# Optimization experiments

Measured on AMD Instinct MI355X. Metric: run time of the kernel, lower is better.

Reference implementation:

```python
import jax, jax.numpy as jnp
import numpy as np

ADJ = np.array([[0,1,0,0,0,0],[1,0,1,0,1,0],[0,1,0,1,0,0],[0,0,1,0,0,0],[0,1,0,0,0,1],[0,0,0,0,1,0]])
EDGES = np.stack(np.nonzero(ADJ), axis=1)  # [10,2] row-major, same order as torch.nonzero
UPPER = (1, 2, 3, 4)
N_PART = 6
B, H, W = 1, 96, 96


def conv1x1(x, w):
    return jnp.einsum('bchw,oc->bohw', x, w)


def affine(x, s, b):  # InPlaceABNSync(activation='none'), eval mode with stats folded into scale/bias
    return x * s[None, :, None, None] + b[None, :, None, None]


def bilinear(x, py, px):  # x [B,C,H,W]; py,px [B,H,W]; zero padding outside
    Hh, Ww = x.shape[2], x.shape[3]
    def samp(img, py, px):
        y0 = jnp.floor(py); x0 = jnp.floor(px)
        wy = py - y0; wx = px - x0
        def get(yi, xi):
            valid = ((yi >= 0) & (yi < Hh) & (xi >= 0) & (xi < Ww)).astype(img.dtype)
            yc = jnp.clip(yi, 0, Hh - 1).astype(jnp.int32)
            xc = jnp.clip(xi, 0, Ww - 1).astype(jnp.int32)
            return img[:, yc, xc] * valid
        return (get(y0, x0) * (1 - wy) * (1 - wx) + get(y0, x0 + 1) * (1 - wy) * wx
                + get(y0 + 1, x0) * wy * (1 - wx) + get(y0 + 1, x0 + 1) * wy * wx)
    return jax.vmap(samp)(x, py, px)


def dfconv(x, ow, ob, w):
    # modulated deformable conv v2 (DCNv2), 3x3, stride 1, pad 1, 1 deformable group
    o = jax.lax.conv_general_dilated(x, ow, (1, 1), 'SAME',
            dimension_numbers=('NCHW', 'OIHW', 'NCHW')) + ob[None, :, None, None]
    off, mask = o[:, :18], jax.nn.sigmoid(o[:, 18:27])
    Hh, Ww = x.shape[2], x.shape[3]
    yy, xx = jnp.meshgrid(jnp.arange(Hh, dtype=x.dtype), jnp.arange(Ww, dtype=x.dtype), indexing='ij')
    out = jnp.zeros((x.shape[0], w.shape[0], Hh, Ww), x.dtype)
    for k in range(9):  # fixed 3x3 taps
        py = yy[None] + (k // 3 - 1) + off[:, 2 * k]
        px = xx[None] + (k % 3 - 1) + off[:, 2 * k + 1]
        s = bilinear(x, py, px) * mask[:, k:k + 1]
        out = out + jnp.einsum('bchw,oc->bohw', s, w[:, :, k // 3, k % 3])
    return out


def gru_cell(x, h, wih, bih, whh, bhh):  # Conv2dGRU cell, 1x1 kernel, single step
    gi = conv1x1(x, wih) + bih[None, :, None, None]
    gh = conv1x1(h, whh) + bhh[None, :, None, None]
    i_r, i_z, i_n = jnp.split(gi, 3, axis=1)
    h_r, h_z, h_n = jnp.split(gh, 3, axis=1)
    r = jax.nn.sigmoid(i_r + h_r)
    z = jax.nn.sigmoid(i_z + h_z)
    n = jnp.tanh(i_n + r * h_n)
    return (1 - z) * n + z * h


def _forward(p_fea, xp, xh, dp_ow1, dp_ob1, dp_w1, dp_s1, dp_b1, dp_ow2, dp_ob2, dp_w2, dp_s2, dp_b2,
             dp_aw, dp_ab, dp_bw, dp_bb, dc_w1, dc_s1, dc_b1, dc_w2, dc_b2, dc_wfh, dc_sfh, dc_bfh,
             gru_wih1, gru_bih1, gru_whh1, gru_bhh1, gru_wih2, gru_bih2, gru_whh2, gru_bhh2):
    # Part_Dependency per directed edge (A -> B)
    per_node = [[] for _ in range(N_PART)]
    for e in range(EDGES.shape[0]):
        a, b = int(EDGES[e, 0]), int(EDGES[e, 1])
        pA, pB = xp[a], xp[b]
        h = jax.nn.relu(affine(dfconv(jnp.concatenate([p_fea, pA], 1), dp_ow1[e], dp_ob1[e], dp_w1[e]), dp_s1[e], dp_b1[e]))
        h = jax.nn.relu(affine(dfconv(h, dp_ow2[e], dp_ob2[e], dp_w2[e]), dp_s2[e], dp_b2[e]))
        A_att = jax.nn.sigmoid(conv1x1(pA, dp_aw[e]) + dp_ab[e][None, :, None, None])
        B_att = jax.nn.sigmoid(conv1x1(pB, dp_bw[e]) + dp_bb[e][None, :, None, None])
        per_node[b].append((1 - A_att) * h * B_att)
    # max-aggregation of incoming messages per part node
    xpp = [m[0] if len(m) == 1 else jnp.max(jnp.stack(m, -1), -1) for m in per_node]
    # decomp: half-node -> part-node messages, then sum
    msgs = []
    for j in range(N_PART):
        hf = xh[0] if (j + 1) in UPPER else xh[1]
        cat = jnp.concatenate([hf, xp[j]], 1)
        a_ = jax.nn.relu(affine(conv1x1(cat, dc_w1[j]), dc_s1[j], dc_b1[j]))
        att = jax.nn.sigmoid(conv1x1(a_, dc_w2[j]) + dc_b2[j][None, :, None, None])
        xhp = jax.nn.relu(affine(conv1x1(att * p_fea, dc_wfh[j]), dc_sfh[j], dc_bfh[j]))
        msgs.append(xpp[j] + xhp)
    # per-node 2-layer Conv2dGRU update (seq len 1, h0 = 0); take layer-2 hidden
    xp_out = []
    h0 = jnp.zeros_like(xp[0])
    for j in range(N_PART):
        xin = jnp.concatenate([xp[j], msgs[j]], 1)
        h1 = gru_cell(xin, h0, gru_wih1[j], gru_bih1[j], gru_whh1[j], gru_bhh1[j])
        h2 = gru_cell(h1, h0, gru_wih2[j], gru_bih2[j], gru_whh2[j], gru_bhh2[j])
        xp_out.append(h2)
    return jnp.stack(xp_out, 0), jnp.stack(msgs, 0)


def setup_inputs():
    ks = iter(jax.random.split(jax.random.key(0), 64))
    nrm = lambda shape, s: jax.random.normal(next(ks), shape, jnp.float32) * s
    HD, IN, E = 10, 256, EDGES.shape[0]
    N = N_PART
    return {
        'p_fea': nrm((B, IN, H, W), 1.0),
        'xp': nrm((N, B, HD, H, W), 1.0),
        'xh': nrm((2, B, HD, H, W), 1.0),
        'dp_ow1': nrm((E, 27, IN + HD, 3, 3), 0.005), 'dp_ob1': nrm((E, 27), 0.01),
        'dp_w1': nrm((E, 2 * HD, IN + HD, 3, 3), 0.02),
        'dp_s1': jnp.ones((E, 2 * HD), jnp.float32), 'dp_b1': jnp.zeros((E, 2 * HD), jnp.float32),
        'dp_ow2': nrm((E, 27, 2 * HD, 3, 3), 0.02), 'dp_ob2': nrm((E, 27), 0.01),
        'dp_w2': nrm((E, HD, 2 * HD, 3, 3), 0.07),
        'dp_s2': jnp.ones((E, HD), jnp.float32), 'dp_b2': jnp.zeros((E, HD), jnp.float32),
        'dp_aw': nrm((E, 1, HD), 0.3), 'dp_ab': jnp.zeros((E, 1), jnp.float32),
        'dp_bw': nrm((E, 1, HD), 0.3), 'dp_bb': jnp.zeros((E, 1), jnp.float32),
        'dc_w1': nrm((N, 2 * HD, 2 * HD), 0.2),
        'dc_s1': jnp.ones((N, 2 * HD), jnp.float32), 'dc_b1': jnp.zeros((N, 2 * HD), jnp.float32),
        'dc_w2': nrm((N, 1, 2 * HD), 0.2), 'dc_b2': jnp.zeros((N, 1), jnp.float32),
        'dc_wfh': nrm((N, HD, IN), 0.06),
        'dc_sfh': jnp.ones((N, HD), jnp.float32), 'dc_bfh': jnp.zeros((N, HD), jnp.float32),
        'gru_wih1': nrm((N, 3 * HD, 2 * HD), 0.2), 'gru_bih1': jnp.zeros((N, 3 * HD), jnp.float32),
        'gru_whh1': nrm((N, 3 * HD, HD), 0.3), 'gru_bhh1': jnp.zeros((N, 3 * HD), jnp.float32),
        'gru_wih2': nrm((N, 3 * HD, HD), 0.3), 'gru_bih2': jnp.zeros((N, 3 * HD), jnp.float32),
        'gru_whh2': nrm((N, 3 * HD, HD), 0.3), 'gru_bhh2': jnp.zeros((N, 3 * HD), jnp.float32),
    }


def reference(p_fea, xp, xh, dp_ow1, dp_ob1, dp_w1, dp_s1, dp_b1, dp_ow2, dp_ob2, dp_w2, dp_s2, dp_b2,
              dp_aw, dp_ab, dp_bw, dp_bb, dc_w1, dc_s1, dc_b1, dc_w2, dc_b2, dc_wfh, dc_sfh, dc_bfh,
              gru_wih1, gru_bih1, gru_whh1, gru_bhh1, gru_wih2, gru_bih2, gru_whh2, gru_bhh2):
    return _forward(p_fea, xp, xh, dp_ow1, dp_ob1, dp_w1, dp_s1, dp_b1, dp_ow2, dp_ob2, dp_w2, dp_s2, dp_b2,
                    dp_aw, dp_ab, dp_bw, dp_bb, dc_w1, dc_s1, dc_b1, dc_w2, dc_b2, dc_wfh, dc_sfh, dc_bfh,
                    gru_wih1, gru_bih1, gru_whh1, gru_bhh1, gru_wih2, gru_bih2, gru_whh2, gru_bhh2)
```

## Files before the change

### kernel.cpp

```cpp
#include <hip/hip_runtime.h>
#include <hip/hip_bf16.h>

#define DEV static __device__ __forceinline__

DEV float sigm(float x) { return 1.f / (1.f + __expf(-x)); }

typedef __attribute__((ext_vector_type(8))) short s8;
typedef __attribute__((ext_vector_type(4))) float f4;
typedef _Float16 h4 __attribute__((ext_vector_type(4)));

DEV unsigned short f2bf(float f) {
  unsigned u = __float_as_uint(f);
  return (unsigned short)((u + 0x7FFFu + ((u >> 16) & 1u)) >> 16);
}
DEV float bf2f(unsigned short h) { return __uint_as_float(((unsigned)h) << 16); }

__constant__ int d_esrc[10] = {0,1,1,1,2,2,3,4,4,5};
__constant__ int d_inc[6][3] = {{1,-1,-1},{0,4,7},{2,6,-1},{5,-1,-1},{3,9,-1},{8,-1,-1}};
__constant__ int d_ne[6] = {1,3,2,1,2,1};

#define TW 32
#define TH 8
#define SW 41
#define SDC 40
#define SH 16
#define SN 656

DEV void prep_w_body(const float* src, float* dst, int OC, int C,
                     int tap_major, int total, int i) {
  if (i >= total) return;
  int t = i % 9; int n = i / 9;
  int c = n % C; n /= C;
  int oc = n % OC; int e = n / OC;
  float v = src[i];
  int inner = tap_major ? (t * C + c) : (c * 9 + t);
  dst[(e * C * 9 + inner) * OC + oc] = v;
}

__global__ void prep_all_k(const float* __restrict__ dp_ow2, float* __restrict__ wf2,
                           const float* __restrict__ dp_w2, float* __restrict__ wm2,
                           const float* __restrict__ dp_ow1,
                           unsigned short* __restrict__ aw1,
                           const float* __restrict__ dp_w1,
                           unsigned short* __restrict__ awY,
                           unsigned short* __restrict__ awU, int use_u) {
  int b = blockIdx.x;
  if (b < 190) {
    prep_w_body(dp_ow2, wf2, 27, 20, 0, 48600, b * 256 + threadIdx.x);
  } else if (b < 261) {
    prep_w_body(dp_w2, wm2, 10, 20, 1, 18000, (b - 190) * 256 + threadIdx.x);
  } else if (b < 926) {
    if (use_u) return;
    int i = (b - 261) * 256 + threadIdx.x;
    if (i >= 170240) return;
    int lane = i & 63;
    int tile = (i >> 6) & 1;
    int cg = (i >> 7) % 133;
    int e = (i >> 7) / 133;
    int m = lane & 15, quad = lane >> 4;
    int oc = tile * 16 + m;
    unsigned short* out = aw1 + ((e * 133 + cg) * 2 + tile) * 1024 + lane * 16;
#pragma unroll
    for (int j = 0; j < 8; ++j) {
      int k = quad * 8 + j;
      int csel = k >> 4, t = k & 15;
      int c = 2 * cg + csel;
      float w = (oc < 27 && t < 9) ? dp_ow1[((e * 27 + oc) * 266 + c) * 9 + t] : 0.f;
      unsigned short h = f2bf(w);
      out[j] = h;
      out[8 + j] = f2bf(w - bf2f(h));
    }
  } else if (b < 1196) {
    if (use_u) return;
    int i = (b - 926) * 256 + threadIdx.x;
    int lane = i & 63;
    int grp = i >> 6;
    int mt = grp % 12;
    int ks = (grp / 12) % 9;
    int e = grp / 108;
    int m16 = lane & 15, quad = lane >> 4;
    int M = mt * 16 + m16;
    unsigned short* out = awY + ((e * 9 + ks) * 12 + mt) * 1024 + lane * 16;
#pragma unroll
    for (int j = 0; j < 8; ++j) {
      int c = ks * 32 + quad * 8 + j;
      float w = 0.f;
      if (M < 180 && c < 266) {
        int tap = M / 20, oc = M % 20;
        w = dp_w1[((e * 20 + oc) * 266 + c) * 9 + tap];
      }
      unsigned short h = f2bf(w);
      out[j] = h;
      out[8 + j] = f2bf(w - bf2f(h));
    }
  } else {
    if (!use_u) return;
    int i = (b - 1196) * 256 + threadIdx.x;
    int lane = i & 63;
    int grp = i >> 6;
    int mt = grp % 28;
    int ks = (grp / 28) % 9;
    int e = grp / 252;
    int m16 = lane & 15, quad = lane >> 4;
    int M = mt * 16 + m16;
    unsigned short* out = awU + ((e * 9 + ks) * 28 + mt) * 1024 + lane * 16;
#pragma unroll
    for (int j = 0; j < 8; ++j) {
      int c = ks * 32 + quad * 8 + j;
      float w = 0.f;
      if (c < 266) {
        if (M < 180) {
          int tap = M / 20, oc = M % 20;
          w = dp_w1[((e * 20 + oc) * 266 + c) * 9 + tap];
        } else if (M >= 192 && M < 435) {
          int u = M - 192, tap = u / 27, oc = u % 27;
          w = dp_ow1[((e * 27 + oc) * 266 + c) * 9 + tap];
        }
      }
      unsigned short h = f2bf(w);
      out[j] = h;
      out[8 + j] = f2bf(w - bf2f(h));
    }
  }
}

__global__ __launch_bounds__(256) void xt_k(
    const float* __restrict__ pfea, const float* __restrict__ xp,
    unsigned short* __restrict__ Xt_p, unsigned short* __restrict__ Xt_x) {
  __shared__ unsigned int lds[256][17];
  const int q0 = blockIdx.x * 256, yb = blockIdx.y;
  const int t = threadIdx.x;
  if (yb < 8) {
    const int c0 = yb * 32;
#pragma unroll
    for (int cc = 0; cc < 32; cc += 2) {
      float v0 = pfea[(c0 + cc) * 9216 + q0 + t];
      float v1 = pfea[(c0 + cc + 1) * 9216 + q0 + t];
      lds[t][cc >> 1] = (unsigned)f2bf(v0) | ((unsigned)f2bf(v1) << 16);
    }
    __syncthreads();
    unsigned int* dst = (unsigned int*)(Xt_p + (size_t)(q0 + t) * 256 + c0);
#pragma unroll
    for (int u = 0; u < 16; ++u) dst[u] = lds[t][u];
  } else {
    const int node = yb - 8;
#pragma unroll
    for (int cc = 0; cc < 32; cc += 2) {
      float v0 = (cc < 10) ? xp[(node * 10 + cc) * 9216 + q0 + t] : 0.f;
      float v1 = (cc + 1 < 10) ? xp[(node * 10 + cc + 1) * 9216 + q0 + t] : 0.f;
      lds[t][cc >> 1] = (unsigned)f2bf(v0) | ((unsigned)f2bf(v1) << 16);
    }
    __syncthreads();
    unsigned int* dst = (unsigned int*)(Xt_x + ((size_t)node * 9216 + q0 + t) * 32);
#pragma unroll
    for (int u = 0; u < 16; ++u) dst[u] = lds[t][u];
  }
}

__global__ void init2_k(const float* __restrict__ ob, float* __restrict__ o2,
                        float* __restrict__ h2) {
  int i = blockIdx.x * 256 + threadIdx.x;
  if (i < 2488320) o2[i] = ob[i / 9216];
  else h2[i - 2488320] = 0.f;
}

DEV int stage_goff(int i, int ty0, int tx0) {
  int r = i / SW, cl = i % SW;
  cl = min(cl, SDC - 1);
  int gy = min(max(ty0 - 4 + r, 0), 95);
  int gx = min(max(tx0 - 4 + cl, 0), 95);
  return gy * 96 + gx;
}

__global__ __launch_bounds__(256) void uni_gemm_k(
    const unsigned short* __restrict__ Xt_p,
    const unsigned short* __restrict__ Xt_x,
    const unsigned short* __restrict__ awU, unsigned short* __restrict__ Yg,
    unsigned short* __restrict__ Ug) {
  const int pxg = blockIdx.x, z = blockIdx.y, e = blockIdx.z;
  const int tid = threadIdx.x;
  const int lane = tid & 63, wv = tid >> 6;
  const int quad = lane >> 4, n16 = lane & 15;
  const unsigned short* xtx = Xt_x + (size_t)d_esrc[e] * 9216 * 32;
  const int qbase = pxg * 256 + wv * 64;
  int q[4];
#pragma unroll
  for (int nt = 0; nt < 4; ++nt) q[nt] = qbase + nt * 16 + n16;

  f4 acc[4][4] = {};

  for (int ks = 0; ks < 9; ++ks) {
    s8 Ah[4], Al[4];
#pragma unroll
    for (int mt = 0; mt < 4; ++mt) {
      const unsigned short* ap =
          awU + (((size_t)e * 9 + ks) * 28 + z * 4 + mt) * 1024 + lane * 16;
      Ah[mt] = *(const s8*)ap;
      Al[mt] = *(const s8*)(ap + 8);
    }
    s8 B[4];
    if (ks < 8) {
      const int co = ks * 32 + quad * 8;
#pragma unroll
      for (int nt = 0; nt < 4; ++nt)
        B[nt] = *(const s8*)(Xt_p + (size_t)q[nt] * 256 + co);
    } else {
      const int co = quad * 8;
#pragma unroll
      for (int nt = 0; nt < 4; ++nt)
        B[nt] = *(const s8*)(xtx + (size_t)q[nt] * 32 + co);
    }
#pragma unroll
    for (int nt = 0; nt < 4; ++nt)
#pragma unroll
      for (int mt = 0; mt < 4; ++mt) {
        acc[nt][mt] = __builtin_amdgcn_mfma_f32_16x16x32_bf16(Ah[mt], B[nt], acc[nt][mt], 0, 0, 0);
        acc[nt][mt] = __builtin_amdgcn_mfma_f32_16x16x32_bf16(Al[mt], B[nt], acc[nt][mt], 0, 0, 0);
      }
  }
  _Float16* Yh = (_Float16*)Yg;
  _Float16* Uh = (_Float16*)Ug;
#pragma unroll
  for (int nt = 0; nt < 4; ++nt) {
#pragma unroll
    for (int mt = 0; mt < 4; ++mt) {
      int m0 = (z * 4 + mt) * 16 + quad * 4;
      if (m0 < 180) {
        int tap = m0 / 20, oc0 = m0 - tap * 20;
        h4 v;
#pragma unroll
        for (int r = 0; r < 4; ++r) v[r] = (_Float16)acc[nt][mt][r];
        *(h4*)(Yh + (((size_t)(e * 9 + tap)) * 9216 + q[nt]) * 20 + oc0) = v;
      } else {
#pragma unroll
        for (int r = 0; r < 4; ++r) {
          int m = m0 + r;
          if (m >= 192 && m < 435)
            Uh[((size_t)e * 243 + (m - 192)) * 9216 + q[nt]] = (_Float16)acc[nt][mt][r];
        }
      }
    }
  }
}

__global__ __launch_bounds__(256) void shiftadd_k(
    const unsigned short* __restrict__ Ug, const float* __restrict__ ob,
    float* __restrict__ o1) {
  const int p = blockIdx.x * 256 + threadIdx.x;
  const int e = blockIdx.y;
  const int y = p / 96, x = p % 96;
  const _Float16* Uh = (const _Float16*)Ug;
  float acc[27];
#pragma unroll
  for (int oc = 0; oc < 27; ++oc) acc[oc] = ob[e * 27 + oc];
#pragma unroll
  for (int t = 0; t < 9; ++t) {
    int yy = y + t / 3 - 1, xx = x + t % 3 - 1;
    if (yy >= 0 && yy < 96 && xx >= 0 && xx < 96) {
      int q = yy * 96 + xx;
      const _Float16* up = Uh + ((size_t)e * 243 + t * 27) * 9216 + q;
#pragma unroll
      for (int oc = 0; oc < 27; ++oc)
        acc[oc] += (float)up[oc * 9216];
    }
  }
#pragma unroll
  for (int oc = 0; oc < 27; ++oc) o1[(e * 27 + oc) * 9216 + p] = acc[oc];
}

#define OSWB 35
#define OSEC 384
#define OBUF 896

__global__ __launch_bounds__(256) void offconv1_mfma_k(
    const float* __restrict__ pfea, const float* __restrict__ xp,
    const unsigned short* __restrict__ aw, const float* __restrict__ ob,
    float* __restrict__ o1) {
  __shared__ float sbuf[2][OBUF];
  const int e = blockIdx.x, m = blockIdx.y, z = blockIdx.z;
  const int tid = threadIdx.x;
  const int lane = tid & 63, wv = tid >> 6;
  const int quad = lane >> 4, n16 = lane & 15;
  const int tx0 = (m % 3) * 32, ty0 = (m / 3) * 8;
  const float* xpe = xp + d_esrc[e] * 10 * 9216;
  const int cg_lo = (z * 133) / 4, cg_hi = ((z + 1) * 133) / 4;

  int g[3]; bool oks[3];
#pragma unroll
  for (int i = 0; i < 3; ++i) {
    int s = tid + i * 256;
    int sec = s / OSEC, off = s - sec * OSEC;
    int r = off / OSWB, cl = off % OSWB;
    int gy = ty0 - 1 + r, gx = tx0 - 1 + cl;
    bool ok = (off < 350) && (cl < 34) && (gy >= 0) && (gy < 96) &&
              (gx >= 0) && (gx < 96);
    oks[i] = ok;
    g[i] = sec * 9216 + (ok ? (gy * 96 + gx) : 0);
  }
  if (tid < OBUF - 768) { sbuf[0][768 + tid] = 0.f; sbuf[1][768 + tid] = 0.f; }

  const int tbase = (quad & 1) * 8;
  const int csel = quad >> 1;
  int bdelta[8];
#pragma unroll
  for (int j = 0; j < 8; ++j) {
    int t = tbase + j;
    int dy = t / 3 - 1, dx = t % 3 - 1;
    bdelta[j] = csel * OSEC + dy * OSWB + dx;
  }
  int bidx[4];
#pragma unroll
  for (int nt = 0; nt < 4; ++nt) {
    int r = 2 * wv + (nt >> 1), h = nt & 1;
    bidx[nt] = (r + 1) * OSWB + (h * 16 + n16 + 1);
  }

  f4 acc[4][2] = {};

  int c0 = 2 * cg_lo;
  const float* base = (c0 < 256) ? (pfea + c0 * 9216) : (xpe + (c0 - 256) * 9216);
  float pv0 = oks[0] ? base[g[0]] : 0.f;
  float pv1 = oks[1] ? base[g[1]] : 0.f;
  float pv2 = oks[2] ? base[g[2]] : 0.f;

  int bsel = 0;
  for (int cg = cg_lo; cg < cg_hi; ++cg, bsel ^= 1) {
    float* buf = sbuf[bsel];
    buf[tid] = pv0; buf[tid + 256] = pv1; buf[tid + 512] = pv2;
    if (cg + 1 < cg_hi) {
      int c0n = 2 * (cg + 1);
      const float* nb = (c0n < 256) ? (pfea + c0n * 9216)
                                    : (xpe + (c0n - 256) * 9216);
      pv0 = oks[0] ? nb[g[0]] : 0.f;
      pv1 = oks[1] ? nb[g[1]] : 0.f;
      pv2 = oks[2] ? nb[g[2]] : 0.f;
    }
    const unsigned short* apc = aw + (e * 133 + cg) * 2048 + lane * 16;
    s8 Ah0 = *(const s8*)(apc);
    s8 Al0 = *(const s8*)(apc + 8);
    s8 Ah1 = *(const s8*)(apc + 1024);
    s8 Al1 = *(const s8*)(apc + 1024 + 8);
    __syncthreads();
#pragma unroll
    for (int nt = 0; nt < 4; ++nt) {
      union { s8 v; unsigned short u[8]; } Bh, Bl;
#pragma unroll
      for (int j = 0; j < 8; ++j) {
        float v = buf[bidx[nt] + bdelta[j]];
        unsigned short h = f2bf(v);
        Bh.u[j] = h;
        Bl.u[j] = f2bf(v - bf2f(h));
      }
      acc[nt][0] = __builtin_amdgcn_mfma_f32_16x16x32_bf16(Ah0, Bh.v, acc[nt][0], 0, 0, 0);
      acc[nt][0] = __builtin_amdgcn_mfma_f32_16x16x32_bf16(Ah0, Bl.v, acc[nt][0], 0, 0, 0);
      acc[nt][0] = __builtin_amdgcn_mfma_f32_16x16x32_bf16(Al0, Bh.v, acc[nt][0], 0, 0, 0);
      acc[nt][1] = __builtin_amdgcn_mfma_f32_16x16x32_bf16(Ah1, Bh.v, acc[nt][1], 0, 0, 0);
      acc[nt][1] = __builtin_amdgcn_mfma_f32_16x16x32_bf16(Ah1, Bl.v, acc[nt][1], 0, 0, 0);
      acc[nt][1] = __builtin_amdgcn_mfma_f32_16x16x32_bf16(Al1, Bh.v, acc[nt][1], 0, 0, 0);
    }
  }
#pragma unroll
  for (int nt = 0; nt < 4; ++nt) {
    int y = ty0 + 2 * wv + (nt >> 1);
    int xx = tx0 + (nt & 1) * 16 + n16;
    int p = y * 96 + xx;
#pragma unroll
    for (int t2 = 0; t2 < 2; ++t2)
#pragma unroll
      for (int r = 0; r < 4; ++r) {
        int oc = t2 * 16 + quad * 4 + r;
        if (oc < 27) {
          float v = acc[nt][t2][r];
          if (z == 0) v += ob[e * 27 + oc];
          atomicAdd(&o1[(e * 27 + oc) * 9216 + p], v);
        }
      }
  }
}

__global__ __launch_bounds__(256) void ygemm_k(
    const float* __restrict__ pfea, const float* __restrict__ xp,
    const unsigned short* __restrict__ awY, unsigned short* __restrict__ Yg) {
  const int pxg = blockIdx.x, z = blockIdx.y, e = blockIdx.z;
  const int tid = threadIdx.x;
  const int lane = tid & 63, wv = tid >> 6;
  const int quad = lane >> 4, n16 = lane & 15;
  const float* xpe = xp + d_esrc[e] * 10 * 9216;
  const int qbase = pxg * 256 + wv * 64;

  f4 acc[4][3] = {};

  for (int ks = 0; ks < 9; ++ks) {
    const int cq = ks * 32 + quad * 8;
    s8 Ah[3], Al[3];
#pragma unroll
    for (int mt = 0; mt < 3; ++mt) {
      const unsigned short* ap =
          awY + ((e * 9 + ks) * 12 + z * 3 + mt) * 1024 + lane * 16;
      Ah[mt] = *(const s8*)ap;
      Al[mt] = *(const s8*)(ap + 8);
    }
#pragma unroll
    for (int nt = 0; nt < 4; ++nt) {
      const int q = qbase + nt * 16 + n16;
      union { s8 v; unsigned short u[8]; } Bh, Bl;
#pragma unroll
      for (int j = 0; j < 8; ++j) {
        int c = cq + j;
        float v = 0.f;
        if (c < 256) v = pfea[c * 9216 + q];
        else if (c < 266) v = xpe[(c - 256) * 9216 + q];
        unsigned short h = f2bf(v);
        Bh.u[j] = h;
        Bl.u[j] = f2bf(v - bf2f(h));
      }
#pragma unroll
      for (int mt = 0; mt < 3; ++mt) {
        acc[nt][mt] = __builtin_amdgcn_mfma_f32_16x16x32_bf16(Ah[mt], Bh.v, acc[nt][mt], 0, 0, 0);
        acc[nt][mt] = __builtin_amdgcn_mfma_f32_16x16x32_bf16(Ah[mt], Bl.v, acc[nt][mt], 0, 0, 0);
        acc[nt][mt] = __builtin_amdgcn_mfma_f32_16x16x32_bf16(Al[mt], Bh.v, acc[nt][mt], 0, 0, 0);
      }
    }
  }
  _Float16* Yh = (_Float16*)Yg;
#pragma unroll
  for (int nt = 0; nt < 4; ++nt) {
    const int q = qbase + nt * 16 + n16;
#pragma unroll
    for (int mt = 0; mt < 3; ++mt)
#pragma unroll
      for (int r = 0; r < 4; ++r) {
        int m = z * 48 + mt * 16 + quad * 4 + r;
        if (m < 180) {
          int tap = m / 20, oc = m - tap * 20;
          Yh[((e * 9 + tap) * 9216 + q) * 20 + oc] = (_Float16)acc[nt][mt][r];
        }
      }
  }
}

__global__ __launch_bounds__(256) void dfgather_k(
    const float* __restrict__ o1, const unsigned short* __restrict__ Yg,
    float* __restrict__ h1a) {
  const int p = blockIdx.x * 256 + threadIdx.x;
  const int zt = blockIdx.y, e = blockIdx.z;
  const int y = p / 96, x = p % 96;
  float acc[20];
#pragma unroll
  for (int oc = 0; oc < 20; ++oc) acc[oc] = 0.f;

  const _Float16* Yh = (const _Float16*)Yg;
#pragma unroll
  for (int t = 0; t < 3; ++t) {
    const int k = zt * 3 + t;
    float offy = o1[(e * 27 + 2 * k) * 9216 + p];
    float offx = o1[(e * 27 + 2 * k + 1) * 9216 + p];
    float mk = sigm(o1[(e * 27 + 18 + k) * 9216 + p]);
    float py = (float)(y + k / 3 - 1) + offy;
    float px = (float)(x + k % 3 - 1) + offx;
    float fy = floorf(py), fx = floorf(px);
    float wy = py - fy, wx = px - fx;
    int iy = (int)fy, ix = (int)fx;
    const _Float16* yk = Yh + (size_t)(e * 9 + k) * 9216 * 20;
#pragma unroll
    for (int dy = 0; dy < 2; ++dy)
#pragma unroll
      for (int dx = 0; dx < 2; ++dx) {
        bool ok = (iy + dy >= 0) && (iy + dy < 96) && (ix + dx >= 0) && (ix + dx < 96);
        float cwc = (ok ? mk : 0.f) * (dy ? wy : (1.f - wy)) * (dx ? wx : (1.f - wx));
        int yc = min(max(iy + dy, 0), 95), xc = min(max(ix + dx, 0), 95);
        const h4* yp = (const h4*)(yk + (yc * 96 + xc) * 20);
#pragma unroll
        for (int g = 0; g < 5; ++g) {
          h4 v = yp[g];
#pragma unroll
          for (int u = 0; u < 4; ++u)
            acc[g * 4 + u] = fmaf(cwc, (float)v[u], acc[g * 4 + u]);
        }
      }
  }
#pragma unroll
  for (int oc = 0; oc < 20; ++oc)
    atomicAdd(&h1a[(e * 20 + oc) * 9216 + p], acc[oc]);
}

__global__ __launch_bounds__(256) void offconv2_k(
    const float* __restrict__ h1a, const float* __restrict__ wf,
    const float* __restrict__ s1, const float* __restrict__ b1,
    float* __restrict__ o2) {
  __shared__ float sbuf[2][2 * SN];
  const int e = blockIdx.x, m = blockIdx.y;
  const int c_lo = blockIdx.z * 10;
  const int tid = threadIdx.x;
  const int tx = tid % TW, ty = tid / TW;
  const int tx0 = (m % 3) * TW, ty0 = (m / 3) * TH;
  const int y = ty0 + ty, x = tx0 + tx;
  const int p = y * 96 + x;
  const float* base = h1a + e * 20 * 9216;

  const int g0 = stage_goff(tid, ty0, tx0);
  const int g1 = stage_goff(tid + 256, ty0, tx0);
  const int g2 = (tid < SN - 512) ? stage_goff(tid + 512, ty0, tx0) : 0;

  float vmask[9];
#pragma unroll
  for (int t = 0; t < 9; ++t) {
    int yy = y + t / 3 - 1, xx = x + t % 3 - 1;
    vmask[t] = ((yy >= 0) && (yy < 96) && (xx >= 0) && (xx < 96)) ? 1.f : 0.f;
  }
  const int vbase = (ty + 3) * SW + (tx + 3);

  float acc[27];
#pragma unroll
  for (int oc = 0; oc < 27; ++oc) acc[oc] = 0.f;

  const float* ia = base + c_lo * 9216;
  const float* ib = ia + 9216;
  float pa0 = ia[g0], pa1 = ia[g1], pa2 = (tid < SN - 512) ? ia[g2] : 0.f;
  float pb0 = ib[g0], pb1 = ib[g1], pb2 = (tid < SN - 512) ? ib[g2] : 0.f;

  int bsel = 0;
  for (int c = c_lo; c < c_lo + 10; c += 2, bsel ^= 1) {
    float sa = s1[e * 20 + c], ba = b1[e * 20 + c];
    float sb = s1[e * 20 + c + 1], bb2 = b1[e * 20 + c + 1];
    float* buf = sbuf[bsel];
    buf[tid] = fmaxf(fmaf(sa, pa0, ba), 0.f);
    buf[tid + 256] = fmaxf(fmaf(sa, pa1, ba), 0.f);
    if (tid < SN - 512) buf[tid + 512] = fmaxf(fmaf(sa, pa2, ba), 0.f);
    buf[SN + tid] = fmaxf(fmaf(sb, pb0, bb2), 0.f);
    buf[SN + tid + 256] = fmaxf(fmaf(sb, pb1, bb2), 0.f);
    if (tid < SN - 512) buf[SN + tid + 512] = fmaxf(fmaf(sb, pb2, bb2), 0.f);
    if (c + 2 < c_lo + 10) {
      const float* na = base + (c + 2) * 9216;
      const float* nb = base + (c + 3) * 9216;
      pa0 = na[g0]; pa1 = na[g1]; if (tid < SN - 512) pa2 = na[g2];
      pb0 = nb[g0]; pb1 = nb[g1]; if (tid < SN - 512) pb2 = nb[g2];
    }
    __syncthreads();
#pragma unroll
    for (int cc = 0; cc < 2; ++cc) {
      const float* wc = wf + (e * 20 + c + cc) * 243;
      const float* bp = buf + cc * SN;
#pragma unroll
      for (int t = 0; t < 9; ++t) {
        float v = vmask[t] * bp[vbase + (t / 3) * SW + (t % 3)];
#pragma unroll
        for (int oc = 0; oc < 27; ++oc)
          acc[oc] = fmaf(v, wc[t * 27 + oc], acc[oc]);
      }
    }
  }
#pragma unroll
  for (int oc = 0; oc < 27; ++oc)
    atomicAdd(&o2[(e * 27 + oc) * 9216 + p], acc[oc]);
}

__global__ __launch_bounds__(256) void dfmain2_k(
    const float* __restrict__ h1a, const float* __restrict__ o2,
    const float* __restrict__ wm, const float* __restrict__ s1,
    const float* __restrict__ b1, float* __restrict__ hout) {
  __shared__ float sbuf[2][2 * SN];
  const int e = blockIdx.x, m = blockIdx.y;
  const int c_lo = blockIdx.z * 10;
  const int tid = threadIdx.x;
  const int tx = tid % TW, ty = tid / TW;
  const int tx0 = (m % 3) * TW, ty0 = (m / 3) * TH;
  const int y = ty0 + ty, x = tx0 + tx;
  const int p = y * 96 + x;
  const float* base = h1a + e * 20 * 9216;

  const int g0 = stage_goff(tid, ty0, tx0);
  const int g1 = stage_goff(tid + 256, ty0, tx0);
  const int g2 = (tid < SN - 512) ? stage_goff(tid + 512, ty0, tx0) : 0;

  int iob[9]; float cw[9][4];
  bool oob = false;
#pragma unroll
  for (int k = 0; k < 9; ++k) {
    float offy = o2[(e * 27 + 2 * k) * 9216 + p];
    float offx = o2[(e * 27 + 2 * k + 1) * 9216 + p];
    float mk = sigm(o2[(e * 27 + 18 + k) * 9216 + p]);
    float py = (float)(y + k / 3 - 1) + offy;
    float px = (float)(x + k % 3 - 1) + offx;
    float fy = floorf(py), fx = floorf(px);
    float wy = py - fy, wx = px - fx;
    int iy = (int)fy, ix = (int)fx;
#pragma unroll
    for (int dy = 0; dy < 2; ++dy)
#pragma unroll
      for (int dx = 0; dx < 2; ++dx) {
        bool ok = (iy + dy >= 0) && (iy + dy < 96) && (ix + dx >= 0) && (ix + dx < 96);
        cw[k][dy * 2 + dx] =
            (ok ? mk : 0.f) * (dy ? wy : (1.f - wy)) * (dx ? wx : (1.f - wx));
      }
    int ir = iy - (ty0 - 4), ic = ix - (tx0 - 4);
    oob |= ((unsigned)ir > (unsigned)(SH - 2)) | ((unsigned)ic > (unsigned)(SDC - 2));
    iob[k] = min(max(ir, 0), SH - 2) * SW + min(max(ic, 0), SDC - 2);
  }

  float acc[10];
#pragma unroll
  for (int oc = 0; oc < 10; ++oc) acc[oc] = 0.f;

  const float* ia = base + c_lo * 9216;
  const float* ib = ia + 9216;
  float pa0 = ia[g0], pa1 = ia[g1], pa2 = (tid < SN - 512) ? ia[g2] : 0.f;
  float pb0 = ib[g0], pb1 = ib[g1], pb2 = (tid < SN - 512) ? ib[g2] : 0.f;

  int bsel = 0;
  for (int c = c_lo; c < c_lo + 10; c += 2, bsel ^= 1) {
    float sa = s1[e * 20 + c], ba = b1[e * 20 + c];
    float sb = s1[e * 20 + c + 1], bb2 = b1[e * 20 + c + 1];
    float* buf = sbuf[bsel];
    buf[tid] = fmaxf(fmaf(sa, pa0, ba), 0.f);
    buf[tid + 256] = fmaxf(fmaf(sa, pa1, ba), 0.f);
    if (tid < SN - 512) buf[tid + 512] = fmaxf(fmaf(sa, pa2, ba), 0.f);
    buf[SN + tid] = fmaxf(fmaf(sb, pb0, bb2), 0.f);
    buf[SN + tid + 256] = fmaxf(fmaf(sb, pb1, bb2), 0.f);
    if (tid < SN - 512) buf[SN + tid + 512] = fmaxf(fmaf(sb, pb2, bb2), 0.f);
    if (c + 2 < c_lo + 10) {
      const float* na = base + (c + 2) * 9216;
      const float* nb = base + (c + 3) * 9216;
      pa0 = na[g0]; pa1 = na[g1]; if (tid < SN - 512) pa2 = na[g2];
      pb0 = nb[g0]; pb1 = nb[g1]; if (tid < SN - 512) pb2 = nb[g2];
    }
    __syncthreads();
#pragma unroll
    for (int cc = 0; cc < 2; ++cc) {
      const float* bp = buf + cc * SN;
#pragma unroll
      for (int k = 0; k < 9; ++k) {
        const float* bk = bp + iob[k];
        float sv = cw[k][0] * bk[0] + cw[k][1] * bk[1] +
                   cw[k][2] * bk[SW] + cw[k][3] * bk[SW + 1];
        const float* wc = wm + ((e * 9 + k) * 20 + c + cc) * 10;
#pragma unroll
        for (int oc = 0; oc < 10; ++oc) acc[oc] = fmaf(sv, wc[oc], acc[oc]);
      }
    }
  }

  if (oob) {
#pragma unroll
    for (int oc = 0; oc < 10; ++oc) acc[oc] = 0.f;
    for (int k = 0; k < 9; ++k) {
      float offy = o2[(e * 27 + 2 * k) * 9216 + p];
      float offx = o2[(e * 27 + 2 * k + 1) * 9216 + p];
      float mk = sigm(o2[(e * 27 + 18 + k) * 9216 + p]);
      float py = (float)(y + k / 3 - 1) + offy;
      float px = (float)(x + k % 3 - 1) + offx;
      float fy = floorf(py), fx = floorf(px);
      float wy = py - fy, wx = px - fx;
      int iy = (int)fy, ix = (int)fx;
      int go[4]; float gw[4];
#pragma unroll
      for (int dy = 0; dy < 2; ++dy)
#pragma unroll
        for (int dx = 0; dx < 2; ++dx) {
          bool ok = (iy + dy >= 0) && (iy + dy < 96) && (ix + dx >= 0) && (ix + dx < 96);
          int yc = min(max(iy + dy, 0), 95), xc = min(max(ix + dx, 0), 95);
          go[dy * 2 + dx] = yc * 96 + xc;
          gw[dy * 2 + dx] =
              (ok ? mk : 0.f) * (dy ? wy : (1.f - wy)) * (dx ? wx : (1.f - wx));
        }
      for (int c = c_lo; c < c_lo + 10; ++c) {
        float sc = s1[e * 20 + c], bc = b1[e * 20 + c];
        const float* ptr = base + c * 9216;
        float v0 = fmaxf(fmaf(sc, ptr[go[0]], bc), 0.f);
        float v1 = fmaxf(fmaf(sc, ptr[go[1]], bc), 0.f);
        float v2 = fmaxf(fmaf(sc, ptr[go[2]], bc), 0.f);
        float v3 = fmaxf(fmaf(sc, ptr[go[3]], bc), 0.f);
        float sv = gw[0] * v0 + gw[1] * v1 + gw[2] * v2 + gw[3] * v3;
        const float* wc = wm + ((e * 9 + k) * 20 + c) * 10;
#pragma unroll
        for (int oc = 0; oc < 10; ++oc) acc[oc] = fmaf(sv, wc[oc], acc[oc]);
      }
    }
  }
#pragma unroll
  for (int oc = 0; oc < 10; ++oc)
    atomicAdd(&hout[(e * 10 + oc) * 9216 + p], acc[oc]);
}

__global__ __launch_bounds__(256) void conv_fh_k(
    const float* __restrict__ pfea, const float* __restrict__ wfh,
    float* __restrict__ accfh) {
  const int j = blockIdx.y;
  const int z = blockIdx.z;
  const int p = blockIdx.x * 256 + threadIdx.x;
  const int c_lo = z * 64;
  float acc[10];
#pragma unroll
  for (int c = 0; c < 10; ++c) acc[c] = 0.f;
  for (int ci = c_lo; ci < c_lo + 64; ci += 4) {
    float pv0 = pfea[ci * 9216 + p];
    float pv1 = pfea[(ci + 1) * 9216 + p];
    float pv2 = pfea[(ci + 2) * 9216 + p];
    float pv3 = pfea[(ci + 3) * 9216 + p];
#pragma unroll
    for (int c = 0; c < 10; ++c) {
      acc[c] = fmaf(pv0, wfh[(j * 10 + c) * 256 + ci], acc[c]);
      acc[c] = fmaf(pv1, wfh[(j * 10 + c) * 256 + ci + 1], acc[c]);
      acc[c] = fmaf(pv2, wfh[(j * 10 + c) * 256 + ci + 2], acc[c]);
      acc[c] = fmaf(pv3, wfh[(j * 10 + c) * 256 + ci + 3], acc[c]);
    }
  }
#pragma unroll
  for (int c = 0; c < 10; ++c)
    atomicAdd(&accfh[(j * 10 + c) * 9216 + p], acc[c]);
}

__global__ __launch_bounds__(256) void msggru_k(
    const float* __restrict__ xp, const float* __restrict__ xh,
    const float* __restrict__ h2, const float* __restrict__ accfh,
    const float* __restrict__ s2, const float* __restrict__ b2g,
    const float* __restrict__ aw, const float* __restrict__ ab,
    const float* __restrict__ bw, const float* __restrict__ bb,
    const float* __restrict__ w1, const float* __restrict__ s1,
    const float* __restrict__ b1, const float* __restrict__ w2,
    const float* __restrict__ b2, const float* __restrict__ sfh,
    const float* __restrict__ bfh,
    const float* __restrict__ wih1, const float* __restrict__ bih1,
    const float* __restrict__ bhh1, const float* __restrict__ wih2,
    const float* __restrict__ bih2, const float* __restrict__ bhh2,
    float* __restrict__ out_m, float* __restrict__ out_x) {
  const int j = blockIdx.y;
  const int p = blockIdx.x * 256 + threadIdx.x;
  float xj[10];
#pragma unroll
  for (int c = 0; c < 10; ++c) xj[c] = xp[(j * 10 + c) * 9216 + p];
  float xpp[10];
  int ne = d_ne[j];
  for (int ei = 0; ei < ne; ++ei) {
    int e = d_inc[j][ei];
    int a2 = d_esrc[e];
    float sA = ab[e];
#pragma unroll
    for (int c = 0; c < 10; ++c)
      sA = fmaf(xp[(a2 * 10 + c) * 9216 + p], aw[e * 10 + c], sA);
    float sB = bb[e];
#pragma unroll
    for (int c = 0; c < 10; ++c) sB = fmaf(xj[c], bw[e * 10 + c], sB);
    float f = (1.f - sigm(sA)) * sigm(sB);
#pragma unroll
    for (int c = 0; c < 10; ++c) {
      float raw = h2[(e * 10 + c) * 9216 + p];
      float hv = fmaxf(fmaf(s2[e * 10 + c], raw, b2g[e * 10 + c]), 0.f);
      float mm = f * hv;
      xpp[c] = (ei == 0) ? mm : fmaxf(xpp[c], mm);
    }
  }
  const float* hf = xh + ((j < 4) ? 0 : 1) * 10 * 9216;
  float cat[20];
#pragma unroll
  for (int c = 0; c < 10; ++c) cat[c] = hf[c * 9216 + p];
#pragma unroll
  for (int c = 0; c < 10; ++c) cat[10 + c] = xj[c];
  float at = b2[j];
#pragma unroll
  for (int oc = 0; oc < 20; ++oc) {
    float t = 0.f;
#pragma unroll
    for (int c = 0; c < 20; ++c)
      t = fmaf(cat[c], w1[(j * 20 + oc) * 20 + c], t);
    float av = fmaxf(s1[j * 20 + oc] * t + b1[j * 20 + oc], 0.f);
    at = fmaf(av, w2[j * 20 + oc], at);
  }
  at = sigm(at);
  float msg[10];
#pragma unroll
  for (int c = 0; c < 10; ++c) {
    float xhp = fmaxf(sfh[j * 10 + c] * (at * accfh[(j * 10 + c) * 9216 + p]) +
                          bfh[j * 10 + c], 0.f);
    msg[c] = xpp[c] + xhp;
    out_m[(j * 10 + c) * 9216 + p] = msg[c];
  }
  float gi[30];
#pragma unroll
  for (int r = 0; r < 30; ++r) gi[r] = bih1[j * 30 + r];
#pragma unroll
  for (int c = 0; c < 10; ++c) {
    float v = xj[c];
#pragma unroll
    for (int r = 0; r < 30; ++r)
      gi[r] = fmaf(v, wih1[(j * 30 + r) * 20 + c], gi[r]);
  }
#pragma unroll
  for (int c = 0; c < 10; ++c) {
    float v = msg[c];
#pragma unroll
    for (int r = 0; r < 30; ++r)
      gi[r] = fmaf(v, wih1[(j * 30 + r) * 20 + 10 + c], gi[r]);
  }
  float h1v[10];
#pragma unroll
  for (int c = 0; c < 10; ++c) {
    float r = sigm(gi[c] + bhh1[j * 30 + c]);
    float z = sigm(gi[10 + c] + bhh1[j * 30 + 10 + c]);
    float n = tanhf(gi[20 + c] + r * bhh1[j * 30 + 20 + c]);
    h1v[c] = (1.f - z) * n;
  }
  float g2v[30];
#pragma unroll
  for (int r = 0; r < 30; ++r) g2v[r] = bih2[j * 30 + r];
#pragma unroll
  for (int c = 0; c < 10; ++c) {
    float v = h1v[c];
#pragma unroll
    for (int r = 0; r < 30; ++r)
      g2v[r] = fmaf(v, wih2[(j * 30 + r) * 10 + c], g2v[r]);
  }
#pragma unroll
  for (int c = 0; c < 10; ++c) {
    float r = sigm(g2v[c] + bhh2[j * 30 + c]);
    float z = sigm(g2v[10 + c] + bhh2[j * 30 + 10 + c]);
    float n = tanhf(g2v[20 + c] + r * bhh2[j * 30 + 20 + c]);
    out_x[(j * 10 + c) * 9216 + p] = (1.f - z) * n;
  }
}

extern "C" void kernel_launch(void* const* d_in, const int* in_sizes, int n_in,
                              void* d_out, int out_size, void* d_ws, size_t ws_size,
                              hipStream_t stream) {
  const float* pfea   = (const float*)d_in[0];
  const float* xp     = (const float*)d_in[1];
  const float* xh     = (const float*)d_in[2];
  const float* dp_ow1 = (const float*)d_in[3];
  const float* dp_ob1 = (const float*)d_in[4];
  const float* dp_w1  = (const float*)d_in[5];
  const float* dp_s1  = (const float*)d_in[6];
  const float* dp_b1  = (const float*)d_in[7];
  const float* dp_ow2 = (const float*)d_in[8];
  const float* dp_ob2 = (const float*)d_in[9];
  const float* dp_w2  = (const float*)d_in[10];
  const float* dp_s2  = (const float*)d_in[11];
  const float* dp_b2  = (const float*)d_in[12];
  const float* dp_aw  = (const float*)d_in[13];
  const float* dp_ab  = (const float*)d_in[14];
  const float* dp_bw  = (const float*)d_in[15];
  const float* dp_bb  = (const float*)d_in[16];
  const float* dc_w1  = (const float*)d_in[17];
  const float* dc_s1  = (const float*)d_in[18];
  const float* dc_b1  = (const float*)d_in[19];
  const float* dc_w2  = (const float*)d_in[20];
  const float* dc_b2  = (const float*)d_in[21];
  const float* dc_wfh = (const float*)d_in[22];
  const float* dc_sfh = (const float*)d_in[23];
  const float* dc_bfh = (const float*)d_in[24];
  const float* g_wih1 = (const float*)d_in[25];
  const float* g_bih1 = (const float*)d_in[26];
  const float* g_bhh1 = (const float*)d_in[28];
  const float* g_wih2 = (const float*)d_in[29];
  const float* g_bih2 = (const float*)d_in[30];
  const float* g_bhh2 = (const float*)d_in[32];

  float* ws = (float*)d_ws;
  const bool use_u = ws_size >= 26654760ull * sizeof(float);

  unsigned short *aw1, *awY = nullptr, *awU = nullptr, *Yg, *Ug = nullptr;
  unsigned short *Xt_p = nullptr, *Xt_x = nullptr;
  float *accfh, *h2, *wf2, *wm2, *o1, *o2, *h1a;

  if (use_u) {
    aw1   = (unsigned short*)ws;
    accfh = ws;
    h2    = ws + 552960;
    awU   = (unsigned short*)(ws + 1474560);
    wf2   = ws + 1474560 + 1290240;
    wm2   = wf2 + 48600;
    o1    = wm2 + 18000;
    o2    = o1;
    Xt_p  = (unsigned short*)o1;
    Xt_x  = Xt_p + 2359296;
    h1a   = o1 + 2488320;
    Yg    = (unsigned short*)(h1a + 1843200);
    Ug    = (unsigned short*)(h1a + 1843200 + 8294400);
  } else {
    aw1   = (unsigned short*)ws;
    awY   = (unsigned short*)(ws + 1361920);
    accfh = ws;
    h2    = ws + 552960;
    wf2   = ws + 1914880;
    wm2   = wf2 + 48600;
    o1    = wm2 + 18000;
    o2    = o1;
    h1a   = o1 + 2488320;
    Yg    = (unsigned short*)(ws + 6313000);
  }

  float* out_x = (float*)d_out;
  float* out_m = out_x + 552960;

  dim3 blk(256);
  prep_all_k<<<dim3(1826), blk, 0, stream>>>(dp_ow2, wf2, dp_w2, wm2,
                                             dp_ow1, aw1, dp_w1, awY ? awY : aw1,
                                             awU ? awU : aw1, use_u ? 1 : 0);

  if (use_u) {
    xt_k<<<dim3(36, 14), blk, 0, stream>>>(pfea, xp, Xt_p, Xt_x);
    hipMemsetAsync(h1a, 0, 1843200 * sizeof(float), stream);
    uni_gemm_k<<<dim3(36, 7, 10), blk, 0, stream>>>(Xt_p, Xt_x, awU, Yg, Ug);
    shiftadd_k<<<dim3(36, 10), blk, 0, stream>>>(Ug, dp_ob1, o1);
    dfgather_k<<<dim3(36, 3, 10), blk, 0, stream>>>(o1, Yg, h1a);
  } else {
    hipMemsetAsync(o1, 0, (2488320 + 1843200) * sizeof(float), stream);
    offconv1_mfma_k<<<dim3(10, 36, 4), blk, 0, stream>>>(pfea, xp, aw1, dp_ob1, o1);
    ygemm_k<<<dim3(36, 4, 10), blk, 0, stream>>>(pfea, xp, awY, Yg);
    dfgather_k<<<dim3(36, 3, 10), blk, 0, stream>>>(o1, Yg, h1a);
  }

  init2_k<<<dim3(13320), blk, 0, stream>>>(dp_ob2, o2, h2);
  offconv2_k<<<dim3(10, 36, 2), blk, 0, stream>>>(h1a, wf2, dp_s1, dp_b1, o2);
  dfmain2_k<<<dim3(10, 36, 2), blk, 0, stream>>>(h1a, o2, wm2, dp_s1, dp_b1, h2);

  hipMemsetAsync(accfh, 0, 552960 * sizeof(float), stream);
  conv_fh_k<<<dim3(36, 6, 4), blk, 0, stream>>>(pfea, dc_wfh, accfh);

  msggru_k<<<dim3(36, 6), blk, 0, stream>>>(
      xp, xh, h2, accfh, dp_s2, dp_b2, dp_aw, dp_ab, dp_bw, dp_bb,
      dc_w1, dc_s1, dc_b1, dc_w2, dc_b2, dc_sfh, dc_bfh,
      g_wih1, g_bih1, g_bhh1, g_wih2, g_bih2, g_bhh2, out_m, out_x);
}
```

Baseline: 396.5 us.

## Store Y as oc-group planes per pixel and drop low-part weight MFMAs

```diff
diff --git a/kernel.cpp b/kernel.cpp
--- a/kernel.cpp
+++ b/kernel.cpp
@@ -190,13 +190,12 @@
   f4 acc[4][4] = {};
 
   for (int ks = 0; ks < 9; ++ks) {
-    s8 Ah[4], Al[4];
+    s8 Ah[4];
 #pragma unroll
     for (int mt = 0; mt < 4; ++mt) {
       const unsigned short* ap =
           awU + (((size_t)e * 9 + ks) * 28 + z * 4 + mt) * 1024 + lane * 16;
       Ah[mt] = *(const s8*)ap;
-      Al[mt] = *(const s8*)(ap + 8);
     }
     s8 B[4];
     if (ks < 8) {
@@ -213,12 +212,10 @@
 #pragma unroll
     for (int nt = 0; nt < 4; ++nt)
 #pragma unroll
-      for (int mt = 0; mt < 4; ++mt) {
+      for (int mt = 0; mt < 4; ++mt)
         acc[nt][mt] = __builtin_amdgcn_mfma_f32_16x16x32_bf16(Ah[mt], B[nt], acc[nt][mt], 0, 0, 0);
-        acc[nt][mt] = __builtin_amdgcn_mfma_f32_16x16x32_bf16(Al[mt], B[nt], acc[nt][mt], 0, 0, 0);
-      }
-  }
-  _Float16* Yh = (_Float16*)Yg;
+  }
+  h4* Y4 = (h4*)Yg;
   _Float16* Uh = (_Float16*)Ug;
 #pragma unroll
   for (int nt = 0; nt < 4; ++nt) {
@@ -226,11 +223,11 @@
     for (int mt = 0; mt < 4; ++mt) {
       int m0 = (z * 4 + mt) * 16 + quad * 4;
       if (m0 < 180) {
-        int tap = m0 / 20, oc0 = m0 - tap * 20;
+        int tap = m0 / 20, ocg = (m0 - tap * 20) >> 2;
         h4 v;
 #pragma unroll
         for (int r = 0; r < 4; ++r) v[r] = (_Float16)acc[nt][mt][r];
-        *(h4*)(Yh + (((size_t)(e * 9 + tap)) * 9216 + q[nt]) * 20 + oc0) = v;
+        Y4[((size_t)(e * 9 + tap) * 5 + ocg) * 9216 + q[nt]] = v;
       } else {
 #pragma unroll
         for (int r = 0; r < 4; ++r) {
@@ -422,20 +419,21 @@
       }
     }
   }
-  _Float16* Yh = (_Float16*)Yg;
+  h4* Y4 = (h4*)Yg;
 #pragma unroll
   for (int nt = 0; nt < 4; ++nt) {
     const int q = qbase + nt * 16 + n16;
 #pragma unroll
-    for (int mt = 0; mt < 3; ++mt)
-#pragma unroll
-      for (int r = 0; r < 4; ++r) {
-        int m = z * 48 + mt * 16 + quad * 4 + r;
-        if (m < 180) {
-          int tap = m / 20, oc = m - tap * 20;
-          Yh[((e * 9 + tap) * 9216 + q) * 20 + oc] = (_Float16)acc[nt][mt][r];
-        }
-      }
+    for (int mt = 0; mt < 3; ++mt) {
+      int m0 = z * 48 + mt * 16 + quad * 4;
+      if (m0 < 180) {
+        int tap = m0 / 20, ocg = (m0 - tap * 20) >> 2;
+        h4 v;
+#pragma unroll
+        for (int r = 0; r < 4; ++r) v[r] = (_Float16)acc[nt][mt][r];
+        Y4[((size_t)(e * 9 + tap) * 5 + ocg) * 9216 + q] = v;
+      }
+    }
   }
 }
 
@@ -449,7 +447,7 @@
 #pragma unroll
   for (int oc = 0; oc < 20; ++oc) acc[oc] = 0.f;
 
-  const _Float16* Yh = (const _Float16*)Yg;
+  const h4* Y4 = (const h4*)Yg;
 #pragma unroll
   for (int t = 0; t < 3; ++t) {
     const int k = zt * 3 + t;
@@ -461,7 +459,7 @@
     float fy = floorf(py), fx = floorf(px);
     float wy = py - fy, wx = px - fx;
     int iy = (int)fy, ix = (int)fx;
-    const _Float16* yk = Yh + (size_t)(e * 9 + k) * 9216 * 20;
+    const h4* yk = Y4 + (size_t)(e * 9 + k) * 5 * 9216;
 #pragma unroll
     for (int dy = 0; dy < 2; ++dy)
 #pragma unroll
@@ -469,10 +467,10 @@
         bool ok = (iy + dy >= 0) && (iy + dy < 96) && (ix + dx >= 0) && (ix + dx < 96);
         float cwc = (ok ? mk : 0.f) * (dy ? wy : (1.f - wy)) * (dx ? wx : (1.f - wx));
         int yc = min(max(iy + dy, 0), 95), xc = min(max(ix + dx, 0), 95);
-        const h4* yp = (const h4*)(yk + (yc * 96 + xc) * 20);
+        int q = yc * 96 + xc;
 #pragma unroll
         for (int g = 0; g < 5; ++g) {
-          h4 v = yp[g];
+          h4 v = yk[g * 9216 + q];
 #pragma unroll
           for (int u = 0; u < 4; ++u)
             acc[g * 4 + u] = fmaf(cwc, (float)v[u], acc[g * 4 + u]);
```

Measured after the change: 462.4 us. 1.17x slower.
